# Kernel tuning notes

Hardware: AMD Instinct MI355X
Metric: run time of the kernel (lower is better)

## Reference

```python
import jax, jax.numpy as jnp
import numpy as np

NUM_HEADS = 8
NUM_GROUPS = 32
EPS = 1e-5


def setup_inputs() -> dict:
    key = jax.random.key(0)
    ks = jax.random.split(key, 12)
    B, C, H, W = 8, 512, 32, 32
    E = 512
    s = 1.0 / np.sqrt(C)
    inp = {
        "input_tensor": jax.random.normal(ks[0], (B, C, H, W), dtype=jnp.float32),
        "Wq": jax.random.normal(ks[1], (C, E), dtype=jnp.float32) * s,
        "bq": jnp.zeros((E,), dtype=jnp.float32),
        "Wk": jax.random.normal(ks[2], (C, E), dtype=jnp.float32) * s,
        "bk": jnp.zeros((E,), dtype=jnp.float32),
        "Wv": jax.random.normal(ks[3], (C, E), dtype=jnp.float32) * s,
        "bv": jnp.zeros((E,), dtype=jnp.float32),
        "Wo": jax.random.normal(ks[4], (E, E), dtype=jnp.float32) * s,
        "bo": jnp.zeros((E,), dtype=jnp.float32),
        "gamma": jnp.ones((E,), dtype=jnp.float32),
        "beta": jnp.zeros((E,), dtype=jnp.float32),
    }
    return inp


def reference(input_tensor, Wq, bq, Wk, bk, Wv, bv, Wo, bo, gamma, beta):
    B, C, H, W = input_tensor.shape
    E = Wq.shape[1]
    nH = NUM_HEADS
    hd = E // nH
    S = H * W

    # [B, C, H, W] -> [B, S, C]
    x = input_tensor.reshape(B, C, S).transpose(0, 2, 1)

    q = (x @ Wq + bq).reshape(B, S, nH, hd).transpose(0, 2, 1, 3)  # [B, h, S, d]
    k = (x @ Wk + bk).reshape(B, S, nH, hd).transpose(0, 2, 1, 3)
    v = (x @ Wv + bv).reshape(B, S, nH, hd).transpose(0, 2, 1, 3)

    scale = hd ** (-0.5)
    scores = jnp.einsum("bhqd,bhkd->bhqk", q, k) * scale
    weights = jax.nn.softmax(scores, axis=-1)
    attn = jnp.einsum("bhqk,bhkd->bhqd", weights, v)  # [B, h, S, d]

    attn = attn.transpose(0, 2, 1, 3).reshape(B, S, E)
    out = attn @ Wo + bo  # [B, S, E]
    out = out.transpose(0, 2, 1).reshape(B, E, H, W)

    y = out + input_tensor

    # GroupNorm over (channels_per_group, H, W)
    G = NUM_GROUPS
    yg = y.reshape(B, G, E // G, H, W)
    mean = jnp.mean(yg, axis=(2, 3, 4), keepdims=True)
    var = jnp.var(yg, axis=(2, 3, 4), keepdims=True)
    yn = ((yg - mean) * jax.lax.rsqrt(var + EPS)).reshape(B, E, H, W)
    return yn * gamma[None, :, None, None] + beta[None, :, None, None]
```

## Files before the change

### kernel.cpp

```cpp
#include <hip/hip_runtime.h>
#include <math.h>

constexpr int Bn  = 8;
constexpr int Cc  = 512;
constexpr int Ss  = 1024;
constexpr int Ee  = 512;
constexpr int nHd = 8;
constexpr int Hd  = 64;
constexpr int Gg  = 32;
constexpr int Cpg = 16;

typedef __bf16 bf16x8 __attribute__((ext_vector_type(8)));
typedef float  f32x4  __attribute__((ext_vector_type(4)));
typedef float  f32x16 __attribute__((ext_vector_type(16)));

__device__ inline __bf16 cvt_bf16(float f) {
    unsigned u = __builtin_bit_cast(unsigned, f);
    u += 0x7fffu + ((u >> 16) & 1u);
    unsigned short h = (unsigned short)(u >> 16);
    return __builtin_bit_cast(__bf16, h);
}

__device__ inline void gld16(const __bf16* g, __bf16* l) {
    __builtin_amdgcn_global_load_lds(
        (const __attribute__((address_space(1))) void*)g,
        (__attribute__((address_space(3))) void*)l, 16, 0, 0);
}

__device__ inline unsigned pk_bf16_rtz(float hi, float lo) {
    return __builtin_amdgcn_perm(__builtin_bit_cast(unsigned, hi),
                                 __builtin_bit_cast(unsigned, lo), 0x07060302u);
}

__global__ __launch_bounds__(256) void transpose_xw(
    const float* __restrict__ x, __bf16* __restrict__ xt,
    const float* __restrict__ w0, const float* __restrict__ w1,
    const float* __restrict__ w2, const float* __restrict__ w3,
    __bf16* __restrict__ d0, __bf16* __restrict__ d1,
    __bf16* __restrict__ d2, __bf16* __restrict__ d3)
{
    __shared__ float T[32][33];
    const int r8 = threadIdx.x >> 5, c32 = threadIdx.x & 31;
    const int z = blockIdx.z;
    if (z < 8) {
        const int b = z, c0 = blockIdx.y * 32, s0 = blockIdx.x * 32;
#pragma unroll
        for (int i = 0; i < 4; i++)
            T[r8 + i * 8][c32] =
                x[((size_t)b * Cc + c0 + r8 + i * 8) * Ss + s0 + c32];
        __syncthreads();
#pragma unroll
        for (int i = 0; i < 4; i++)
            xt[((size_t)b * Ss + s0 + r8 + i * 8) * Cc + c0 + c32] =
                cvt_bf16(T[c32][r8 + i * 8]);
    } else {
        if (blockIdx.x >= 16) return;
        const int m = z - 8;
        const float* src = (m == 0) ? w0 : (m == 1) ? w1 : (m == 2) ? w2 : w3;
        __bf16* dst = (m == 0) ? d0 : (m == 1) ? d1 : (m == 2) ? d2 : d3;
        const int e0 = blockIdx.x * 32, c0 = blockIdx.y * 32;
#pragma unroll
        for (int i = 0; i < 4; i++)
            T[r8 + i * 8][c32] = src[(size_t)(c0 + r8 + i * 8) * Ee + e0 + c32];
        __syncthreads();
#pragma unroll
        for (int i = 0; i < 4; i++)
            dst[(size_t)(e0 + r8 + i * 8) * Cc + c0 + c32] =
                cvt_bf16(T[c32][r8 + i * 8]);
    }
}

__global__ __launch_bounds__(256) void qkv_mfma(
    const __bf16* __restrict__ xt,
    const __bf16* __restrict__ wqt, const __bf16* __restrict__ wkt,
    const __bf16* __restrict__ wvt,
    const float* __restrict__ bq, const float* __restrict__ bk,
    const float* __restrict__ bv,
    __bf16* __restrict__ qb, __bf16* __restrict__ kb, __bf16* __restrict__ vt)
{
    const int b = blockIdx.z;
    const int wsel = blockIdx.y >> 2;
    const int e0 = (blockIdx.y & 3) * 128;
    const int s0 = blockIdx.x * 128;
    const __bf16* A  = xt + (size_t)b * Ss * Cc;
    const __bf16* Bm = (wsel == 0) ? wqt : (wsel == 1) ? wkt : wvt;
    const float*  bias = (wsel == 0) ? bq : (wsel == 1) ? bk : bv;

    __shared__ __align__(16) char smem[128 * 136 * 2];
    __bf16* As = (__bf16*)smem;
    __bf16* Bs = (__bf16*)(smem + 8192);
    __bf16* T  = (__bf16*)smem;

    const int wave = threadIdx.x >> 6, lane = threadIdx.x & 63;
    const int lid = lane & 15, quad = lane >> 4;
    const int wm = wave & 1, wn = wave >> 1;
    const int srow = lane >> 2, sch = lane & 3;

    f32x4 acc[4][4] = {};

    for (int k0 = 0; k0 < Cc; k0 += 32) {
#pragma unroll
        for (int i = 0; i < 2; i++) {
            const int inst = wave * 2 + i;
            const int r = inst * 16 + srow;
            gld16(&A [(size_t)(s0 + r) * Cc + k0 + sch * 8], &As[inst * 512]);
            gld16(&Bm[(size_t)(e0 + r) * Cc + k0 + sch * 8], &Bs[inst * 512]);
        }
        __syncthreads();
        bf16x8 af[4], bf[4];
#pragma unroll
        for (int i = 0; i < 4; i++)
            af[i] = *(const bf16x8*)&As[(wm * 64 + i * 16 + lid) * 32 + quad * 8];
#pragma unroll
        for (int j = 0; j < 4; j++)
            bf[j] = *(const bf16x8*)&Bs[(wn * 64 + j * 16 + lid) * 32 + quad * 8];
#pragma unroll
        for (int i = 0; i < 4; i++)
#pragma unroll
            for (int j = 0; j < 4; j++)
                acc[i][j] = __builtin_amdgcn_mfma_f32_16x16x32_bf16(
                    af[i], bf[j], acc[i][j], 0, 0, 0);
        __syncthreads();
    }

    float bj[4];
#pragma unroll
    for (int j = 0; j < 4; j++) bj[j] = bias[e0 + wn * 64 + j * 16 + lid];

    if (wsel == 2) {
#pragma unroll
        for (int i = 0; i < 4; i++) {
            const int s4 = wm * 64 + i * 16 + quad * 4;
#pragma unroll
            for (int j = 0; j < 4; j++) {
                const int e_l = wn * 64 + j * 16 + lid;
                unsigned short u0 = __builtin_bit_cast(unsigned short, cvt_bf16(acc[i][j][0] + bj[j]));
                unsigned short u1 = __builtin_bit_cast(unsigned short, cvt_bf16(acc[i][j][1] + bj[j]));
                unsigned short u2 = __builtin_bit_cast(unsigned short, cvt_bf16(acc[i][j][2] + bj[j]));
                unsigned short u3 = __builtin_bit_cast(unsigned short, cvt_bf16(acc[i][j][3] + bj[j]));
                uint2 pk;
                pk.x = (unsigned)u0 | ((unsigned)u1 << 16);
                pk.y = (unsigned)u2 | ((unsigned)u3 << 16);
                *(uint2*)&T[e_l * 136 + s4] = pk;
            }
        }
        __syncthreads();
        const int t = threadIdx.x;
#pragma unroll
        for (int it = 0; it < 8; it++) {
            const int idx = t + it * 256;
            const int e_l = idx >> 4, c8 = (idx & 15) * 8;
            bf16x8 val = *(const bf16x8*)&T[e_l * 136 + c8];
            const int e_g = e0 + e_l;
            const int head = e_g >> 6, d = e_g & 63;
            *(bf16x8*)&vt[(((size_t)b * nHd + head) * Hd + d) * Ss + s0 + c8] = val;
        }
    } else {
        __bf16* outp = (wsel == 0) ? qb : kb;
#pragma unroll
        for (int i = 0; i < 4; i++) {
#pragma unroll
            for (int j = 0; j < 4; j++) {
                const int e1 = e0 + wn * 64 + j * 16 + lid;
                const int head = e1 >> 6, d = e1 & 63;
#pragma unroll
                for (int r = 0; r < 4; r++) {
                    const int s1 = s0 + wm * 64 + i * 16 + quad * 4 + r;
                    outp[(((size_t)b * nHd + head) * Ss + s1) * Hd + d] =
                        cvt_bf16(acc[i][j][r] + bj[j]);
                }
            }
        }
    }
}

__global__ __launch_bounds__(256, 2) void attn_mfma(
    const __bf16* __restrict__ q, const __bf16* __restrict__ k,
    const __bf16* __restrict__ vt, __bf16* __restrict__ attn_out)
{
    const int bh = blockIdx.x;
    const int s0 = blockIdx.y * 128;
    const __bf16* qp = q  + (size_t)bh * Ss * Hd;
    const __bf16* kp = k  + (size_t)bh * Ss * Hd;
    const __bf16* vp = vt + (size_t)bh * Hd * Ss;

    __shared__ __align__(16) __bf16 Ks[128 * 64];
    __shared__ __align__(16) __bf16 Vs[64 * 128];
    __shared__ __align__(16) __bf16 Ps[4][32 * 128];

    const int wave = threadIdx.x >> 6, lane = threadIdx.x & 63;
    const int nl = lane & 31, h = lane >> 5;
    __bf16* PsW = Ps[wave];

    const int sq = s0 + wave * 32 + nl;
    bf16x8 qf[4];
#pragma unroll
    for (int kk2 = 0; kk2 < 4; kk2++)
        qf[kk2] = *(const bf16x8*)&qp[(size_t)sq * Hd + kk2 * 16 + h * 8];

    f32x16 oacc[2] = {};
    float rs = 0.0f;
    const float cexp = 0.125f * 1.44269504f;

    const int srow8 = lane >> 3, sch8 = lane & 7;
    const int srow4 = lane >> 4, sch16 = lane & 15;

    for (int kt = 0; kt < 8; kt++) {
#pragma unroll
        for (int i = 0; i < 4; i++) {
            const int inst = wave * 4 + i;
            const int rK = inst * 8 + srow8;
            gld16(&kp[(size_t)(kt * 128 + rK) * Hd + ((sch8 ^ (rK & 7)) * 8)],
                  &Ks[inst * 512]);
            const int dR = inst * 4 + srow4;
            gld16(&vp[(size_t)dR * Ss + kt * 128 + ((sch16 ^ (dR & 15)) * 8)],
                  &Vs[inst * 512]);
        }
        __syncthreads();

        f32x16 sc[4] = {};
#pragma unroll
        for (int kk2 = 0; kk2 < 4; kk2++) {
#pragma unroll
            for (int mt = 0; mt < 4; mt++) {
                bf16x8 kf = *(const bf16x8*)&Ks[(mt * 32 + nl) * 64 +
                                                (((2 * kk2 + h) ^ (nl & 7)) * 8)];
                sc[mt] = __builtin_amdgcn_mfma_f32_32x32x16_bf16(
                    kf, qf[kk2], sc[mt], 0, 0, 0);
            }
        }

#pragma unroll
        for (int mt = 0; mt < 4; mt++) {
            float p[16];
#pragma unroll
            for (int r = 0; r < 16; r++) {
                p[r] = __builtin_amdgcn_exp2f(sc[mt][r] * cexp);
                rs += p[r];
            }
#pragma unroll
            for (int g = 0; g < 4; g++) {
                uint2 pk;
                pk.x = pk_bf16_rtz(p[4 * g + 1], p[4 * g + 0]);
                pk.y = pk_bf16_rtz(p[4 * g + 3], p[4 * g + 2]);
                const int gr = (mt * 8 + 2 * g + h) ^ ((nl & 15) << 1);
                *(uint2*)&PsW[nl * 128 + gr * 4] = pk;
            }
        }

#pragma unroll
        for (int kk = 0; kk < 8; kk++) {
            const int cp = (kk * 2 + h) ^ (nl & 15);
            bf16x8 pf = *(const bf16x8*)&PsW[nl * 128 + cp * 8];
#pragma unroll
            for (int dt = 0; dt < 2; dt++) {
                bf16x8 vf = *(const bf16x8*)&Vs[(dt * 32 + nl) * 128 +
                                                (((kk * 2 + h) ^ (nl & 15)) * 8)];
                oacc[dt] = __builtin_amdgcn_mfma_f32_32x32x16_bf16(
                    pf, vf, oacc[dt], 0, 0, 0);
            }
        }
        __syncthreads();
    }

    rs += __shfl_xor(rs, 32, 64);
    const float inv = 1.0f / rs;
    const int b = bh >> 3, head = bh & 7;
#pragma unroll
    for (int r = 0; r < 16; r++) {
        const int rowq = (r & 3) + 8 * (r >> 2) + 4 * h;
        const float invr = __shfl(inv, rowq, 64);
        const int s1 = s0 + wave * 32 + rowq;
#pragma unroll
        for (int dt = 0; dt < 2; dt++)
            attn_out[((size_t)b * Ss + s1) * Ee + head * Hd + dt * 32 + nl] =
                cvt_bf16(oacc[dt][r] * invr);
    }
}

__global__ __launch_bounds__(256) void outproj_mfma(
    const __bf16* __restrict__ attnb, const __bf16* __restrict__ wot,
    const float* __restrict__ bo, const float* __restrict__ xin,
    __bf16* __restrict__ y)
{
    const int b  = blockIdx.z;
    const int e0 = blockIdx.y * 128;
    const int s0 = blockIdx.x * 128;
    const __bf16* Bm = attnb + (size_t)b * Ss * Ee;

    __shared__ __align__(16) __bf16 As[128 * 32];
    __shared__ __align__(16) __bf16 Bs[128 * 32];

    const int wave = threadIdx.x >> 6, lane = threadIdx.x & 63;
    const int lid = lane & 15, quad = lane >> 4;
    const int wm = wave & 1, wn = wave >> 1;
    const int srow = lane >> 2, sch = lane & 3;

    f32x4 acc[4][4] = {};

    for (int k0 = 0; k0 < Ee; k0 += 32) {
#pragma unroll
        for (int i = 0; i < 2; i++) {
            const int inst = wave * 2 + i;
            const int r = inst * 16 + srow;
            gld16(&wot[(size_t)(e0 + r) * Ee + k0 + sch * 8], &As[inst * 512]);
            gld16(&Bm [(size_t)(s0 + r) * Ee + k0 + sch * 8], &Bs[inst * 512]);
        }
        __syncthreads();
        bf16x8 af[4], bf[4];
#pragma unroll
        for (int i = 0; i < 4; i++)
            af[i] = *(const bf16x8*)&As[(wm * 64 + i * 16 + lid) * 32 + quad * 8];
#pragma unroll
        for (int j = 0; j < 4; j++)
            bf[j] = *(const bf16x8*)&Bs[(wn * 64 + j * 16 + lid) * 32 + quad * 8];
#pragma unroll
        for (int i = 0; i < 4; i++)
#pragma unroll
            for (int j = 0; j < 4; j++)
                acc[i][j] = __builtin_amdgcn_mfma_f32_16x16x32_bf16(
                    af[i], bf[j], acc[i][j], 0, 0, 0);
        __syncthreads();
    }

#pragma unroll
    for (int i = 0; i < 4; i++) {
#pragma unroll
        for (int r = 0; r < 4; r++) {
            const int eo1 = e0 + wm * 64 + i * 16 + quad * 4 + r;
            const float bb = bo[eo1];
#pragma unroll
            for (int j = 0; j < 4; j++) {
                const int s1 = s0 + wn * 64 + j * 16 + lid;
                const size_t idx = ((size_t)b * Ee + eo1) * Ss + s1;
                y[idx] = cvt_bf16(acc[i][j][r] + bb + xin[idx]);
            }
        }
    }
}

__global__ __launch_bounds__(256) void gnorm_kernel(
    const __bf16* __restrict__ y, const float* __restrict__ gamma,
    const float* __restrict__ beta, float* __restrict__ out)
{
    const int bg = blockIdx.x;
    const int b = bg >> 5, g = bg & 31;
    const size_t base = ((size_t)b * Ee + g * Cpg) * Ss;
    const bf16x8* y8 = (const bf16x8*)(y + base);
    constexpr int N8 = (Cpg * Ss) / 8;

    float s = 0.f, s2 = 0.f;
    for (int i = threadIdx.x; i < N8; i += 256) {
        bf16x8 vv = y8[i];
#pragma unroll
        for (int j = 0; j < 8; j++) {
            const float f = (float)vv[j];
            s += f; s2 += f * f;
        }
    }
#pragma unroll
    for (int off = 32; off > 0; off >>= 1) {
        s  += __shfl_down(s, off, 64);
        s2 += __shfl_down(s2, off, 64);
    }
    __shared__ float red[8];
    __shared__ float stats[2];
    const int lane = threadIdx.x & 63, wid = threadIdx.x >> 6;
    if (lane == 0) { red[wid] = s; red[4 + wid] = s2; }
    __syncthreads();
    if (threadIdx.x == 0) {
        float ts  = red[0] + red[1] + red[2] + red[3];
        float ts2 = red[4] + red[5] + red[6] + red[7];
        float mean = ts / (float)(Cpg * Ss);
        float var  = ts2 / (float)(Cpg * Ss) - mean * mean;
        stats[0] = mean;
        stats[1] = rsqrtf(var + 1e-5f);
    }
    __syncthreads();
    const float mean = stats[0], rstd = stats[1];
    for (int i = threadIdx.x; i < N8; i += 256) {
        bf16x8 vv = y8[i];
        const int c = g * Cpg + (i >> 7);
        const float gm = gamma[c] * rstd;
        const float bt = beta[c];
        f32x4 r0, r1;
#pragma unroll
        for (int j = 0; j < 4; j++) r0[j] = ((float)vv[j] - mean) * gm + bt;
#pragma unroll
        for (int j = 0; j < 4; j++) r1[j] = ((float)vv[4 + j] - mean) * gm + bt;
        *(f32x4*)&out[base + (size_t)i * 8]     = r0;
        *(f32x4*)&out[base + (size_t)i * 8 + 4] = r1;
    }
}

extern "C" void kernel_launch(void* const* d_in, const int* in_sizes, int n_in,
                              void* d_out, int out_size, void* d_ws, size_t ws_size,
                              hipStream_t stream)
{
    const float* x     = (const float*)d_in[0];
    const float* Wq    = (const float*)d_in[1];
    const float* bq    = (const float*)d_in[2];
    const float* Wk    = (const float*)d_in[3];
    const float* bk    = (const float*)d_in[4];
    const float* Wv    = (const float*)d_in[5];
    const float* bv    = (const float*)d_in[6];
    const float* Wo    = (const float*)d_in[7];
    const float* bo    = (const float*)d_in[8];
    const float* gamma = (const float*)d_in[9];
    const float* beta  = (const float*)d_in[10];
    float* out = (float*)d_out;

    char* ws = (char*)d_ws;
    __bf16* xt    = (__bf16*)ws;
    __bf16* wqt   = (__bf16*)(ws + (8u << 20));
    __bf16* wkt   = (__bf16*)(ws + (8u << 20) + (512u << 10));
    __bf16* wvt   = (__bf16*)(ws + (9u << 20));
    __bf16* wot   = (__bf16*)(ws + (9u << 20) + (512u << 10));
    __bf16* qb    = (__bf16*)(ws + (10u << 20));
    __bf16* kb    = (__bf16*)(ws + (18u << 20));
    __bf16* vtb   = (__bf16*)(ws + (26u << 20));
    __bf16* attnb = (__bf16*)(ws + (34u << 20));
    __bf16* yb    = (__bf16*)(ws + (42u << 20));

    transpose_xw<<<dim3(32, 16, 12), 256, 0, stream>>>(
        x, xt, Wq, Wk, Wv, Wo, wqt, wkt, wvt, wot);

    qkv_mfma<<<dim3(Ss / 128, 12, Bn), 256, 0, stream>>>(
        xt, wqt, wkt, wvt, bq, bk, bv, qb, kb, vtb);

    attn_mfma<<<dim3(Bn * nHd, Ss / 128), 256, 0, stream>>>(qb, kb, vtb, attnb);

    outproj_mfma<<<dim3(Ss / 128, Ee / 128, Bn), 256, 0, stream>>>(
        attnb, wot, bo, x, yb);

    gnorm_kernel<<<Bn * Gg, 256, 0, stream>>>(yb, gamma, beta, out);
}
```

Measured before the change: 161.4 us.

## Keep softmax probabilities in registers and fuse GroupNorm statistics into out-projection

The attention kernel no longer stages the bf16 probability tile through per-wave shared memory. It builds the MFMA A-operand fragments directly in registers, using cross-half lane shuffles, which removes the LDS writes and reads and frees 32KB of shared memory per block. Separately, the out-projection epilogue now accumulates per-group sum and sum-of-squares and adds them into a stats buffer with atomics. That buffer is zeroed in the transpose kernel, so the GroupNorm kernel skips its first full read pass of y. The cost is extra shuffles and float atomics, whose accumulation order is nondeterministic.

Measured after the change: 164.1 us. Within noise of the previous version (+1.7%).

```diff
diff --git a/kernel.cpp b/kernel.cpp
--- a/kernel.cpp
+++ b/kernel.cpp
@@ -13,6 +13,7 @@
 typedef __bf16 bf16x8 __attribute__((ext_vector_type(8)));
 typedef float  f32x4  __attribute__((ext_vector_type(4)));
 typedef float  f32x16 __attribute__((ext_vector_type(16)));
+typedef unsigned u32x4 __attribute__((ext_vector_type(4)));
 
 __device__ inline __bf16 cvt_bf16(float f) {
     unsigned u = __builtin_bit_cast(unsigned, f);
@@ -37,7 +38,8 @@
     const float* __restrict__ w0, const float* __restrict__ w1,
     const float* __restrict__ w2, const float* __restrict__ w3,
     __bf16* __restrict__ d0, __bf16* __restrict__ d1,
-    __bf16* __restrict__ d2, __bf16* __restrict__ d3)
+    __bf16* __restrict__ d2, __bf16* __restrict__ d3,
+    float* __restrict__ stats)
 {
     __shared__ float T[32][33];
     const int r8 = threadIdx.x >> 5, c32 = threadIdx.x & 31;
@@ -54,6 +56,10 @@
             xt[((size_t)b * Ss + s0 + r8 + i * 8) * Cc + c0 + c32] =
                 cvt_bf16(T[c32][r8 + i * 8]);
     } else {
+        if (z == 8 && blockIdx.x == 0 && blockIdx.y == 0) {
+            stats[threadIdx.x] = 0.0f;
+            stats[threadIdx.x + 256] = 0.0f;
+        }
         if (blockIdx.x >= 16) return;
         const int m = z - 8;
         const float* src = (m == 0) ? w0 : (m == 1) ? w1 : (m == 2) ? w2 : w3;
@@ -186,11 +192,9 @@
 
     __shared__ __align__(16) __bf16 Ks[128 * 64];
     __shared__ __align__(16) __bf16 Vs[64 * 128];
-    __shared__ __align__(16) __bf16 Ps[4][32 * 128];
 
     const int wave = threadIdx.x >> 6, lane = threadIdx.x & 63;
     const int nl = lane & 31, h = lane >> 5;
-    __bf16* PsW = Ps[wave];
 
     const int sq = s0 + wave * 32 + nl;
     bf16x8 qf[4];
@@ -230,6 +234,7 @@
             }
         }
 
+        unsigned frag[8][4];
 #pragma unroll
         for (int mt = 0; mt < 4; mt++) {
             float p[16];
@@ -238,20 +243,34 @@
                 p[r] = __builtin_amdgcn_exp2f(sc[mt][r] * cexp);
                 rs += p[r];
             }
-#pragma unroll
-            for (int g = 0; g < 4; g++) {
-                uint2 pk;
-                pk.x = pk_bf16_rtz(p[4 * g + 1], p[4 * g + 0]);
-                pk.y = pk_bf16_rtz(p[4 * g + 3], p[4 * g + 2]);
-                const int gr = (mt * 8 + 2 * g + h) ^ ((nl & 15) << 1);
-                *(uint2*)&PsW[nl * 128 + gr * 4] = pk;
-            }
+            unsigned G[4][2];
+#pragma unroll
+            for (int qg = 0; qg < 4; qg++) {
+                G[qg][0] = pk_bf16_rtz(p[4 * qg + 1], p[4 * qg + 0]);
+                G[qg][1] = pk_bf16_rtz(p[4 * qg + 3], p[4 * qg + 2]);
+            }
+            const unsigned sA0 = h ? G[0][0] : G[1][0];
+            const unsigned sA1 = h ? G[0][1] : G[1][1];
+            const unsigned sB0 = h ? G[2][0] : G[3][0];
+            const unsigned sB1 = h ? G[2][1] : G[3][1];
+            const unsigned rA0 = __shfl_xor(sA0, 32, 64);
+            const unsigned rA1 = __shfl_xor(sA1, 32, 64);
+            const unsigned rB0 = __shfl_xor(sB0, 32, 64);
+            const unsigned rB1 = __shfl_xor(sB1, 32, 64);
+            frag[2 * mt][0]     = h ? rA0     : G[0][0];
+            frag[2 * mt][1]     = h ? rA1     : G[0][1];
+            frag[2 * mt][2]     = h ? G[1][0] : rA0;
+            frag[2 * mt][3]     = h ? G[1][1] : rA1;
+            frag[2 * mt + 1][0] = h ? rB0     : G[2][0];
+            frag[2 * mt + 1][1] = h ? rB1     : G[2][1];
+            frag[2 * mt + 1][2] = h ? G[3][0] : rB0;
+            frag[2 * mt + 1][3] = h ? G[3][1] : rB1;
         }
 
 #pragma unroll
         for (int kk = 0; kk < 8; kk++) {
-            const int cp = (kk * 2 + h) ^ (nl & 15);
-            bf16x8 pf = *(const bf16x8*)&PsW[nl * 128 + cp * 8];
+            u32x4 fv = {frag[kk][0], frag[kk][1], frag[kk][2], frag[kk][3]};
+            bf16x8 pf = __builtin_bit_cast(bf16x8, fv);
 #pragma unroll
             for (int dt = 0; dt < 2; dt++) {
                 bf16x8 vf = *(const bf16x8*)&Vs[(dt * 32 + nl) * 128 +
@@ -281,7 +300,7 @@
 __global__ __launch_bounds__(256) void outproj_mfma(
     const __bf16* __restrict__ attnb, const __bf16* __restrict__ wot,
     const float* __restrict__ bo, const float* __restrict__ xin,
-    __bf16* __restrict__ y)
+    __bf16* __restrict__ y, float* __restrict__ stats)
 {
     const int b  = blockIdx.z;
     const int e0 = blockIdx.y * 128;
@@ -323,6 +342,7 @@
         __syncthreads();
     }
 
+    float gs[4] = {}, gs2[4] = {};
 #pragma unroll
     for (int i = 0; i < 4; i++) {
 #pragma unroll
@@ -333,51 +353,45 @@
             for (int j = 0; j < 4; j++) {
                 const int s1 = s0 + wn * 64 + j * 16 + lid;
                 const size_t idx = ((size_t)b * Ee + eo1) * Ss + s1;
-                y[idx] = cvt_bf16(acc[i][j][r] + bb + xin[idx]);
-            }
+                const float v = acc[i][j][r] + bb + xin[idx];
+                y[idx] = cvt_bf16(v);
+                gs[i]  += v;
+                gs2[i] += v * v;
+            }
+        }
+    }
+#pragma unroll
+    for (int i = 0; i < 4; i++) {
+        float a = gs[i], c = gs2[i];
+#pragma unroll
+        for (int off = 32; off > 0; off >>= 1) {
+            a += __shfl_down(a, off, 64);
+            c += __shfl_down(c, off, 64);
+        }
+        if (lane == 0) {
+            const int g = (e0 >> 4) + wm * 4 + i;
+            atomicAdd(&stats[(b * Gg + g) * 2 + 0], a);
+            atomicAdd(&stats[(b * Gg + g) * 2 + 1], c);
         }
     }
 }
 
 __global__ __launch_bounds__(256) void gnorm_kernel(
     const __bf16* __restrict__ y, const float* __restrict__ gamma,
-    const float* __restrict__ beta, float* __restrict__ out)
+    const float* __restrict__ beta, const float* __restrict__ stats,
+    float* __restrict__ out)
 {
     const int bg = blockIdx.x;
     const int b = bg >> 5, g = bg & 31;
     const size_t base = ((size_t)b * Ee + g * Cpg) * Ss;
     const bf16x8* y8 = (const bf16x8*)(y + base);
     constexpr int N8 = (Cpg * Ss) / 8;
-
-    float s = 0.f, s2 = 0.f;
-    for (int i = threadIdx.x; i < N8; i += 256) {
-        bf16x8 vv = y8[i];
-#pragma unroll
-        for (int j = 0; j < 8; j++) {
-            const float f = (float)vv[j];
-            s += f; s2 += f * f;
-        }
-    }
-#pragma unroll
-    for (int off = 32; off > 0; off >>= 1) {
-        s  += __shfl_down(s, off, 64);
-        s2 += __shfl_down(s2, off, 64);
-    }
-    __shared__ float red[8];
-    __shared__ float stats[2];
-    const int lane = threadIdx.x & 63, wid = threadIdx.x >> 6;
-    if (lane == 0) { red[wid] = s; red[4 + wid] = s2; }
-    __syncthreads();
-    if (threadIdx.x == 0) {
-        float ts  = red[0] + red[1] + red[2] + red[3];
-        float ts2 = red[4] + red[5] + red[6] + red[7];
-        float mean = ts / (float)(Cpg * Ss);
-        float var  = ts2 / (float)(Cpg * Ss) - mean * mean;
-        stats[0] = mean;
-        stats[1] = rsqrtf(var + 1e-5f);
-    }
-    __syncthreads();
-    const float mean = stats[0], rstd = stats[1];
+    constexpr float Nf = (float)(Cpg * Ss);
+
+    const float mean = stats[bg * 2 + 0] / Nf;
+    const float var  = stats[bg * 2 + 1] / Nf - mean * mean;
+    const float rstd = rsqrtf(var + 1e-5f);
+
     for (int i = threadIdx.x; i < N8; i += 256) {
         bf16x8 vv = y8[i];
         const int c = g * Cpg + (i >> 7);
@@ -421,9 +435,10 @@
     __bf16* vtb   = (__bf16*)(ws + (26u << 20));
     __bf16* attnb = (__bf16*)(ws + (34u << 20));
     __bf16* yb    = (__bf16*)(ws + (42u << 20));
+    float*  statb = (float*) (ws + (50u << 20));
 
     transpose_xw<<<dim3(32, 16, 12), 256, 0, stream>>>(
-        x, xt, Wq, Wk, Wv, Wo, wqt, wkt, wvt, wot);
+        x, xt, Wq, Wk, Wv, Wo, wqt, wkt, wvt, wot, statb);
 
     qkv_mfma<<<dim3(Ss / 128, 12, Bn), 256, 0, stream>>>(
         xt, wqt, wkt, wvt, bq, bk, bv, qb, kb, vtb);
@@ -431,7 +446,7 @@
     attn_mfma<<<dim3(Bn * nHd, Ss / 128), 256, 0, stream>>>(qb, kb, vtb, attnb);
 
     outproj_mfma<<<dim3(Ss / 128, Ee / 128, Bn), 256, 0, stream>>>(
-        attnb, wot, bo, x, yb);
-
-    gnorm_kernel<<<Bn * Gg, 256, 0, stream>>>(yb, gamma, beta, out);
-}
+        attnb, wot, bo, x, yb, statb);
+
+    gnorm_kernel<<<Bn * Gg, 256, 0, stream>>>(yb, gamma, beta, statb, out);
+}
```
